# Kernel tuning notes

Hardware: AMD Instinct MI355X
Metric: run time of the kernel (lower is better)

The kernel has to match this reference:

```python
import jax, jax.numpy as jnp
import numpy as np
import math

B, H, L, DK = 2, 8, 2048, 64
SQRT_TERMS = 3  # 1 + tree + leaf_PE


def setup_inputs() -> dict:
    key = jax.random.key(0)
    ks = jax.random.split(key, 6)
    query = jax.random.normal(ks[0], (B, H, L, DK), dtype=jnp.float32)
    k = jax.random.normal(ks[1], (B, H, L, DK), dtype=jnp.float32)
    value = jax.random.normal(ks[2], (B, H, L, DK), dtype=jnp.float32)
    mask = jax.random.randint(ks[3], (B, 1, L, L), 0, 2).astype(jnp.bool_)
    tree_score = jax.random.normal(ks[4], (B, H, L, L), dtype=jnp.float32)
    leaf_score = jax.random.normal(ks[5], (B, H, L, L), dtype=jnp.float32)
    return {"query": query, "key": k, "value": value, "mask": mask,
            "tree_score": tree_score, "leaf_score": leaf_score}


def reference(query, key, value, mask, tree_score, leaf_score):
    # w_score = QK^T + tree bias + leaf bias, scaled by sqrt(3 * d_k)
    w_score = jnp.einsum('bhik,bhjk->bhij', query, key)
    w_score = (w_score + tree_score + leaf_score) / math.sqrt(SQRT_TERMS * query.shape[-1])
    # masked_fill(mask, -1e9): mask==True positions are suppressed
    w_score = jnp.where(mask, jnp.float32(-1e9), w_score)
    p_attn = jax.nn.softmax(w_score, axis=-1)
    attn_sum = jnp.einsum('bhij,bhjk->bhik', p_attn, value)
    return (attn_sum, p_attn)
```

## Files before the change

### kernel.cpp

```cpp
#include <hip/hip_runtime.h>


#define B_   2
#define H_   8
#define L_   2048
#define DK_  64
#define BH_  16
#define M_   16
#define SCALE 0.07216878364870323f
#define MASKVAL -65504.0f

typedef __attribute__((ext_vector_type(8))) short    short8;
typedef __attribute__((ext_vector_type(4))) float    f32x4;
typedef __attribute__((ext_vector_type(4))) int      i32x4;
typedef __attribute__((ext_vector_type(4))) _Float16 h16x4;
typedef __attribute__((ext_vector_type(8))) _Float16 h16x8;

__device__ __forceinline__ unsigned short f2bf(float f) {
    union { float f; unsigned int i; } x; x.f = f;
    unsigned int u = x.i;
    return (unsigned short)((u + 0x7fffu + ((u >> 16) & 1u)) >> 16);
}
__device__ __forceinline__ short8 pack8f(const float* a) {
    short8 r;
#pragma unroll
    for (int i = 0; i < 8; ++i) r[i] = (short)f2bf(a[i]);
    return r;
}
__device__ __forceinline__ int swz(int row, int colByte) {
    return (row * (L_ * 2) + colByte) ^ ((row & 7) << 4);
}

__global__ __launch_bounds__(256)
void raa_fused_kernel(const float* __restrict__ q,
                      const float* __restrict__ k,
                      const float* __restrict__ v,
                      const int*   __restrict__ mask,
                      const float* __restrict__ tree,
                      const float* __restrict__ leaf,
                      float*       __restrict__ attn,
                      float*       __restrict__ p)
{
    const int t    = threadIdx.x;
    const int wv   = t >> 6;
    const int lane = t & 63;
    const int bh   = blockIdx.x;
    const int b    = bh >> 3;
    const int i0   = blockIdx.y * M_;

    __shared__ __align__(16) unsigned short s16[M_ * L_];
    __shared__ float s_m[M_], s_linv[M_];
    char* sb = (char*)s16;

    const int prow = t >> 4;
    const int pc4  = (t & 15) * 4;

    const size_t bias_row = ((size_t)bh * L_ + i0 + prow) * L_ + pc4;
    const size_t mask_row = ((size_t)b  * L_ + i0 + prow) * L_ + pc4;
    f32x4 tB0 = __builtin_nontemporal_load((const f32x4*)(tree + bias_row));
    f32x4 lB0 = __builtin_nontemporal_load((const f32x4*)(leaf + bias_row));
    i32x4 mB0 = *(const i32x4*)(mask + mask_row);
    f32x4 tB1 = __builtin_nontemporal_load((const f32x4*)(tree + bias_row + 64));
    f32x4 lB1 = __builtin_nontemporal_load((const f32x4*)(leaf + bias_row + 64));
    i32x4 mB1 = *(const i32x4*)(mask + mask_row + 64);

    const size_t qbase = ((size_t)bh * L_ + i0 + (lane & 15)) * (size_t)DK_
                       + ((lane >> 4) * 8);
    float qf[8], qg[8];
    *(f32x4*)&qf[0] = *(const f32x4*)(q + qbase);
    *(f32x4*)&qf[4] = *(const f32x4*)(q + qbase + 4);
    *(f32x4*)&qg[0] = *(const f32x4*)(q + qbase + 32);
    *(f32x4*)&qg[4] = *(const f32x4*)(q + qbase + 36);
    const short8 aq0 = pack8f(qf), aq1 = pack8f(qg);

    const float* kbase = k + (size_t)bh * L_ * DK_ + ((lane >> 4) * 8);
    const int kr = wv * 16 + (lane & 15);
    float kc[16];
    {
        const float* kp = kbase + (size_t)kr * DK_;
        *(f32x4*)&kc[0]  = *(const f32x4*)(kp);
        *(f32x4*)&kc[4]  = *(const f32x4*)(kp + 4);
        *(f32x4*)&kc[8]  = *(const f32x4*)(kp + 32);
        *(f32x4*)&kc[12] = *(const f32x4*)(kp + 36);
    }
    for (int jc = 0; jc < 32; ++jc) {
        float kn[16];
        {
            const int nj = (jc < 31) ? jc + 1 : 31;
            const float* kp = kbase + (size_t)(nj * 64 + kr) * DK_;
            *(f32x4*)&kn[0]  = *(const f32x4*)(kp);
            *(f32x4*)&kn[4]  = *(const f32x4*)(kp + 4);
            *(f32x4*)&kn[8]  = *(const f32x4*)(kp + 32);
            *(f32x4*)&kn[12] = *(const f32x4*)(kp + 36);
        }
        const short8 kb0 = pack8f(&kc[0]);
        const short8 kb1 = pack8f(&kc[8]);
        f32x4 acc = {0.f, 0.f, 0.f, 0.f};
        acc = __builtin_amdgcn_mfma_f32_16x16x32_bf16(aq0, kb0, acc, 0, 0, 0);
        acc = __builtin_amdgcn_mfma_f32_16x16x32_bf16(aq1, kb1, acc, 0, 0, 0);
        const int r0   = (lane >> 4) * 4;
        const int ccol = jc * 64 + wv * 16 + (lane & 15);
#pragma unroll
        for (int r = 0; r < 4; ++r)
            *(_Float16*)(sb + swz(r0 + r, ccol * 2)) = (_Float16)acc[r];
#pragma unroll
        for (int u = 0; u < 16; ++u) kc[u] = kn[u];
    }
    __syncthreads();

    float m_loc = -INFINITY, l_loc = 0.f;
    auto procB = [&](int jc, f32x4 t4, f32x4 l4, i32x4 mk) {
        const int ad = swz(prow, (jc * 64 + pc4) * 2);
        h16x4 qh = *(h16x4*)(sb + ad);
        float su[4];
#pragma unroll
        for (int e = 0; e < 4; ++e) {
            float s = ((float)qh[e] + t4[e] + l4[e]) * SCALE;
            s = mk[e] ? MASKVAL : s;
            _Float16 hs = (_Float16)s;
            qh[e] = hs;
            su[e] = (float)hs;
        }
        *(h16x4*)(sb + ad) = qh;
        const float cmax = fmaxf(fmaxf(su[0], su[1]), fmaxf(su[2], su[3]));
        if (cmax > m_loc) { l_loc *= __expf(m_loc - cmax); m_loc = cmax; }
        l_loc += __expf(su[0] - m_loc) + __expf(su[1] - m_loc)
               + __expf(su[2] - m_loc) + __expf(su[3] - m_loc);
    };
    for (int jc = 0; jc < 32; jc += 2) {
        {
            const f32x4 t4 = tB0, l4 = lB0; const i32x4 mk = mB0;
            const int nj = (jc + 2 < 32) ? jc + 2 : jc;
            const size_t off = bias_row + (size_t)nj * 64;
            tB0 = __builtin_nontemporal_load((const f32x4*)(tree + off));
            lB0 = __builtin_nontemporal_load((const f32x4*)(leaf + off));
            mB0 = *(const i32x4*)(mask + mask_row + (size_t)nj * 64);
            procB(jc, t4, l4, mk);
        }
        {
            const f32x4 t4 = tB1, l4 = lB1; const i32x4 mk = mB1;
            const int nj = (jc + 3 < 32) ? jc + 3 : jc + 1;
            const size_t off = bias_row + (size_t)nj * 64;
            tB1 = __builtin_nontemporal_load((const f32x4*)(tree + off));
            lB1 = __builtin_nontemporal_load((const f32x4*)(leaf + off));
            mB1 = *(const i32x4*)(mask + mask_row + (size_t)nj * 64);
            procB(jc + 1, t4, l4, mk);
        }
    }
#pragma unroll
    for (int d = 1; d < 16; d <<= 1) {
        const float mo = __shfl_xor(m_loc, d);
        const float lo = __shfl_xor(l_loc, d);
        const float mn = fmaxf(m_loc, mo);
        l_loc = l_loc * __expf(m_loc - mn) + lo * __expf(mo - mn);
        m_loc = mn;
    }
    if ((t & 15) == 0) { s_m[prow] = m_loc; s_linv[prow] = 1.f / l_loc; }
    __syncthreads();

    {
        const float mrow = s_m[prow], li = s_linv[prow];
        const size_t prowoff = ((size_t)bh * L_ + i0 + prow) * L_;
        const int c8 = (t & 15) * 8;
        for (int ch = 0; ch < 16; ++ch) {
            const int col = ch * 128 + c8;
            const int ad  = swz(prow, col * 2);
            const h16x8 hv = *(const h16x8*)(sb + ad);
            float pv[8];
#pragma unroll
            for (int e = 0; e < 8; ++e) pv[e] = __expf((float)hv[e] - mrow) * li;
            f32x4 o0 = { pv[0], pv[1], pv[2], pv[3] };
            f32x4 o1 = { pv[4], pv[5], pv[6], pv[7] };
            __builtin_nontemporal_store(o0, (f32x4*)(p + prowoff + col));
            __builtin_nontemporal_store(o1, (f32x4*)(p + prowoff + col + 4));
            *(short8*)(sb + ad) = pack8f(pv);
        }
    }
    __syncthreads();

    f32x4 oacc = {0.f, 0.f, 0.f, 0.f};
    const float* vb = v + (size_t)bh * L_ * DK_ + wv * 16 + (lane & 15);
#pragma unroll 2
    for (int ch = 0; ch < 16; ++ch) {
#pragma unroll
        for (int kk = 0; kk < 4; ++kk) {
            const int jb = ch * 128 + kk * 32 + (lane >> 4) * 8;
            const short8 af = *(const short8*)(sb + swz(lane & 15, jb * 2));
            const float* vp = vb + (size_t)jb * DK_;
            float vf[8];
#pragma unroll
            for (int u = 0; u < 8; ++u) vf[u] = vp[(size_t)u * DK_];
            const short8 bfr = pack8f(vf);
            oacc = __builtin_amdgcn_mfma_f32_16x16x32_bf16(af, bfr, oacc, 0, 0, 0);
        }
    }
    {
        const int r0  = (lane >> 4) * 4;
        const int col = wv * 16 + (lane & 15);
#pragma unroll
        for (int r = 0; r < 4; ++r)
            attn[((size_t)bh * L_ + i0 + r0 + r) * DK_ + col] = oacc[r];
    }
}

extern "C" void kernel_launch(void* const* d_in, const int* in_sizes, int n_in,
                              void* d_out, int out_size, void* d_ws, size_t ws_size,
                              hipStream_t stream) {
    const float* q    = (const float*)d_in[0];
    const float* k    = (const float*)d_in[1];
    const float* v    = (const float*)d_in[2];
    const int*   mask = (const int*)d_in[3];
    const float* tree = (const float*)d_in[4];
    const float* leaf = (const float*)d_in[5];

    float* attn = (float*)d_out;
    float* p    = attn + (size_t)B_ * H_ * L_ * DK_;

    dim3 grid(BH_, L_ / M_);
    raa_fused_kernel<<<grid, 256, 0, stream>>>(q, k, v, mask, tree, leaf, attn, p);
}
```

Before: 790.3 us.

## Halve query rows per block and pre-convert K/V to bf16 in workspace

Each block now handles 8 query rows instead of 16, which halves shared memory per block and doubles the grid. It also raises the launch-bounds occupancy hint to 4 blocks. When workspace is available, a separate pre-pass converts K and V to bf16 so the fused kernel reads half-size operands and skips per-block repacking. The cost is that each K/V tile is reread by twice as many blocks, half of every MFMA's rows go unused, and there is an extra kernel launch.

```diff
diff --git a/kernel.cpp b/kernel.cpp
--- a/kernel.cpp
+++ b/kernel.cpp
@@ -6,7 +6,7 @@
 #define L_   2048
 #define DK_  64
 #define BH_  16
-#define M_   16
+#define M_   8
 #define SCALE 0.07216878364870323f
 #define MASKVAL -65504.0f
 
@@ -32,9 +32,25 @@
 }
 
 __global__ __launch_bounds__(256)
+void cvt_kv_bf16(const float* __restrict__ k, const float* __restrict__ v,
+                 unsigned short* __restrict__ out) {
+    const size_t N = (size_t)B_ * H_ * L_ * DK_;
+    const size_t stride = (size_t)gridDim.x * blockDim.x * 8;
+    for (size_t i = ((size_t)blockIdx.x * blockDim.x + threadIdx.x) * 8;
+         i < 2 * N; i += stride) {
+        const float* src = (i < N) ? (k + i) : (v + (i - N));
+        float a[8];
+        *(f32x4*)&a[0] = *(const f32x4*)(src);
+        *(f32x4*)&a[4] = *(const f32x4*)(src + 4);
+        *(short8*)(out + i) = pack8f(a);
+    }
+}
+
+template<bool BF>
+__global__ __launch_bounds__(256, 4)
 void raa_fused_kernel(const float* __restrict__ q,
-                      const float* __restrict__ k,
-                      const float* __restrict__ v,
+                      const void*  __restrict__ kptr,
+                      const void*  __restrict__ vptr,
                       const int*   __restrict__ mask,
                       const float* __restrict__ tree,
                       const float* __restrict__ leaf,
@@ -52,20 +68,21 @@
     __shared__ float s_m[M_], s_linv[M_];
     char* sb = (char*)s16;
 
-    const int prow = t >> 4;
-    const int pc4  = (t & 15) * 4;
+    const int prow = t >> 5;
+    const int lr   = t & 31;
+    const int pc4  = lr * 4;
 
     const size_t bias_row = ((size_t)bh * L_ + i0 + prow) * L_ + pc4;
     const size_t mask_row = ((size_t)b  * L_ + i0 + prow) * L_ + pc4;
     f32x4 tB0 = __builtin_nontemporal_load((const f32x4*)(tree + bias_row));
     f32x4 lB0 = __builtin_nontemporal_load((const f32x4*)(leaf + bias_row));
     i32x4 mB0 = *(const i32x4*)(mask + mask_row);
-    f32x4 tB1 = __builtin_nontemporal_load((const f32x4*)(tree + bias_row + 64));
-    f32x4 lB1 = __builtin_nontemporal_load((const f32x4*)(leaf + bias_row + 64));
-    i32x4 mB1 = *(const i32x4*)(mask + mask_row + 64);
-
-    const size_t qbase = ((size_t)bh * L_ + i0 + (lane & 15)) * (size_t)DK_
-                       + ((lane >> 4) * 8);
+    f32x4 tB1 = __builtin_nontemporal_load((const f32x4*)(tree + bias_row + 128));
+    f32x4 lB1 = __builtin_nontemporal_load((const f32x4*)(leaf + bias_row + 128));
+    i32x4 mB1 = *(const i32x4*)(mask + mask_row + 128);
+
+    const int qrow = (i0 + (lane & 15) < L_) ? i0 + (lane & 15) : L_ - 1;
+    const size_t qbase = ((size_t)bh * L_ + qrow) * (size_t)DK_ + ((lane >> 4) * 8);
     float qf[8], qg[8];
     *(f32x4*)&qf[0] = *(const f32x4*)(q + qbase);
     *(f32x4*)&qf[4] = *(const f32x4*)(q + qbase + 4);
@@ -73,44 +90,77 @@
     *(f32x4*)&qg[4] = *(const f32x4*)(q + qbase + 36);
     const short8 aq0 = pack8f(qf), aq1 = pack8f(qg);
 
-    const float* kbase = k + (size_t)bh * L_ * DK_ + ((lane >> 4) * 8);
     const int kr = wv * 16 + (lane & 15);
-    float kc[16];
-    {
-        const float* kp = kbase + (size_t)kr * DK_;
-        *(f32x4*)&kc[0]  = *(const f32x4*)(kp);
-        *(f32x4*)&kc[4]  = *(const f32x4*)(kp + 4);
-        *(f32x4*)&kc[8]  = *(const f32x4*)(kp + 32);
-        *(f32x4*)&kc[12] = *(const f32x4*)(kp + 36);
-    }
-    for (int jc = 0; jc < 32; ++jc) {
-        float kn[16];
+    const int r0 = (lane >> 4) * 4;
+    if constexpr (BF) {
+        const unsigned short* kb16 = (const unsigned short*)kptr
+                                   + (size_t)bh * L_ * DK_ + ((lane >> 4) * 8);
+        short8 kc0, kc1;
         {
-            const int nj = (jc < 31) ? jc + 1 : 31;
-            const float* kp = kbase + (size_t)(nj * 64 + kr) * DK_;
-            *(f32x4*)&kn[0]  = *(const f32x4*)(kp);
-            *(f32x4*)&kn[4]  = *(const f32x4*)(kp + 4);
-            *(f32x4*)&kn[8]  = *(const f32x4*)(kp + 32);
-            *(f32x4*)&kn[12] = *(const f32x4*)(kp + 36);
-        }
-        const short8 kb0 = pack8f(&kc[0]);
-        const short8 kb1 = pack8f(&kc[8]);
-        f32x4 acc = {0.f, 0.f, 0.f, 0.f};
-        acc = __builtin_amdgcn_mfma_f32_16x16x32_bf16(aq0, kb0, acc, 0, 0, 0);
-        acc = __builtin_amdgcn_mfma_f32_16x16x32_bf16(aq1, kb1, acc, 0, 0, 0);
-        const int r0   = (lane >> 4) * 4;
-        const int ccol = jc * 64 + wv * 16 + (lane & 15);
-#pragma unroll
-        for (int r = 0; r < 4; ++r)
-            *(_Float16*)(sb + swz(r0 + r, ccol * 2)) = (_Float16)acc[r];
-#pragma unroll
-        for (int u = 0; u < 16; ++u) kc[u] = kn[u];
+            const unsigned short* kp = kb16 + (size_t)kr * DK_;
+            kc0 = *(const short8*)(kp);
+            kc1 = *(const short8*)(kp + 32);
+        }
+        for (int jc = 0; jc < 32; ++jc) {
+            short8 kn0, kn1;
+            {
+                const int nj = (jc < 31) ? jc + 1 : 31;
+                const unsigned short* kp = kb16 + (size_t)(nj * 64 + kr) * DK_;
+                kn0 = *(const short8*)(kp);
+                kn1 = *(const short8*)(kp + 32);
+            }
+            f32x4 acc = {0.f, 0.f, 0.f, 0.f};
+            acc = __builtin_amdgcn_mfma_f32_16x16x32_bf16(aq0, kc0, acc, 0, 0, 0);
+            acc = __builtin_amdgcn_mfma_f32_16x16x32_bf16(aq1, kc1, acc, 0, 0, 0);
+            const int ccol = jc * 64 + wv * 16 + (lane & 15);
+            if (r0 < M_) {
+#pragma unroll
+                for (int r = 0; r < 4; ++r)
+                    *(_Float16*)(sb + swz(r0 + r, ccol * 2)) = (_Float16)acc[r];
+            }
+            kc0 = kn0; kc1 = kn1;
+        }
+    } else {
+        const float* kbase = (const float*)kptr + (size_t)bh * L_ * DK_
+                           + ((lane >> 4) * 8);
+        float kc[16];
+        {
+            const float* kp = kbase + (size_t)kr * DK_;
+            *(f32x4*)&kc[0]  = *(const f32x4*)(kp);
+            *(f32x4*)&kc[4]  = *(const f32x4*)(kp + 4);
+            *(f32x4*)&kc[8]  = *(const f32x4*)(kp + 32);
+            *(f32x4*)&kc[12] = *(const f32x4*)(kp + 36);
+        }
+        for (int jc = 0; jc < 32; ++jc) {
+            float kn[16];
+            {
+                const int nj = (jc < 31) ? jc + 1 : 31;
+                const float* kp = kbase + (size_t)(nj * 64 + kr) * DK_;
+                *(f32x4*)&kn[0]  = *(const f32x4*)(kp);
+                *(f32x4*)&kn[4]  = *(const f32x4*)(kp + 4);
+                *(f32x4*)&kn[8]  = *(const f32x4*)(kp + 32);
+                *(f32x4*)&kn[12] = *(const f32x4*)(kp + 36);
+            }
+            const short8 kb0 = pack8f(&kc[0]);
+            const short8 kb1 = pack8f(&kc[8]);
+            f32x4 acc = {0.f, 0.f, 0.f, 0.f};
+            acc = __builtin_amdgcn_mfma_f32_16x16x32_bf16(aq0, kb0, acc, 0, 0, 0);
+            acc = __builtin_amdgcn_mfma_f32_16x16x32_bf16(aq1, kb1, acc, 0, 0, 0);
+            const int ccol = jc * 64 + wv * 16 + (lane & 15);
+            if (r0 < M_) {
+#pragma unroll
+                for (int r = 0; r < 4; ++r)
+                    *(_Float16*)(sb + swz(r0 + r, ccol * 2)) = (_Float16)acc[r];
+            }
+#pragma unroll
+            for (int u = 0; u < 16; ++u) kc[u] = kn[u];
+        }
     }
     __syncthreads();
 
     float m_loc = -INFINITY, l_loc = 0.f;
     auto procB = [&](int jc, f32x4 t4, f32x4 l4, i32x4 mk) {
-        const int ad = swz(prow, (jc * 64 + pc4) * 2);
+        const int ad = swz(prow, (jc * 128 + pc4) * 2);
         h16x4 qh = *(h16x4*)(sb + ad);
         float su[4];
 #pragma unroll
@@ -127,43 +177,43 @@
         l_loc += __expf(su[0] - m_loc) + __expf(su[1] - m_loc)
                + __expf(su[2] - m_loc) + __expf(su[3] - m_loc);
     };
-    for (int jc = 0; jc < 32; jc += 2) {
+    for (int jc = 0; jc < 16; jc += 2) {
         {
             const f32x4 t4 = tB0, l4 = lB0; const i32x4 mk = mB0;
-            const int nj = (jc + 2 < 32) ? jc + 2 : jc;
-            const size_t off = bias_row + (size_t)nj * 64;
+            const int nj = (jc + 2 < 16) ? jc + 2 : jc;
+            const size_t off = bias_row + (size_t)nj * 128;
             tB0 = __builtin_nontemporal_load((const f32x4*)(tree + off));
             lB0 = __builtin_nontemporal_load((const f32x4*)(leaf + off));
-            mB0 = *(const i32x4*)(mask + mask_row + (size_t)nj * 64);
+            mB0 = *(const i32x4*)(mask + mask_row + (size_t)nj * 128);
             procB(jc, t4, l4, mk);
         }
         {
             const f32x4 t4 = tB1, l4 = lB1; const i32x4 mk = mB1;
-            const int nj = (jc + 3 < 32) ? jc + 3 : jc + 1;
-            const size_t off = bias_row + (size_t)nj * 64;
+            const int nj = (jc + 3 < 16) ? jc + 3 : jc + 1;
+            const size_t off = bias_row + (size_t)nj * 128;
             tB1 = __builtin_nontemporal_load((const f32x4*)(tree + off));
             lB1 = __builtin_nontemporal_load((const f32x4*)(leaf + off));
-            mB1 = *(const i32x4*)(mask + mask_row + (size_t)nj * 64);
+            mB1 = *(const i32x4*)(mask + mask_row + (size_t)nj * 128);
             procB(jc + 1, t4, l4, mk);
         }
     }
 #pragma unroll
-    for (int d = 1; d < 16; d <<= 1) {
+    for (int d = 1; d < 32; d <<= 1) {
         const float mo = __shfl_xor(m_loc, d);
         const float lo = __shfl_xor(l_loc, d);
         const float mn = fmaxf(m_loc, mo);
         l_loc = l_loc * __expf(m_loc - mn) + lo * __expf(mo - mn);
         m_loc = mn;
     }
-    if ((t & 15) == 0) { s_m[prow] = m_loc; s_linv[prow] = 1.f / l_loc; }
+    if (lr == 0) { s_m[prow] = m_loc; s_linv[prow] = 1.f / l_loc; }
     __syncthreads();
 
     {
         const float mrow = s_m[prow], li = s_linv[prow];
         const size_t prowoff = ((size_t)bh * L_ + i0 + prow) * L_;
-        const int c8 = (t & 15) * 8;
-        for (int ch = 0; ch < 16; ++ch) {
-            const int col = ch * 128 + c8;
+        const int c8 = lr * 8;
+        for (int ch = 0; ch < 8; ++ch) {
+            const int col = ch * 256 + c8;
             const int ad  = swz(prow, col * 2);
             const h16x8 hv = *(const h16x8*)(sb + ad);
             float pv[8];
@@ -179,27 +229,47 @@
     __syncthreads();
 
     f32x4 oacc = {0.f, 0.f, 0.f, 0.f};
-    const float* vb = v + (size_t)bh * L_ * DK_ + wv * 16 + (lane & 15);
+    if constexpr (BF) {
+        const unsigned short* vb16 = (const unsigned short*)vptr
+                                   + (size_t)bh * L_ * DK_ + wv * 16 + (lane & 15);
 #pragma unroll 2
-    for (int ch = 0; ch < 16; ++ch) {
-#pragma unroll
-        for (int kk = 0; kk < 4; ++kk) {
-            const int jb = ch * 128 + kk * 32 + (lane >> 4) * 8;
-            const short8 af = *(const short8*)(sb + swz(lane & 15, jb * 2));
-            const float* vp = vb + (size_t)jb * DK_;
-            float vf[8];
-#pragma unroll
-            for (int u = 0; u < 8; ++u) vf[u] = vp[(size_t)u * DK_];
-            const short8 bfr = pack8f(vf);
-            oacc = __builtin_amdgcn_mfma_f32_16x16x32_bf16(af, bfr, oacc, 0, 0, 0);
+        for (int ch = 0; ch < 16; ++ch) {
+#pragma unroll
+            for (int kk = 0; kk < 4; ++kk) {
+                const int jb = ch * 128 + kk * 32 + (lane >> 4) * 8;
+                const short8 af = *(const short8*)(sb + swz(lane & 7, jb * 2));
+                const unsigned short* vp = vb16 + (size_t)jb * DK_;
+                short8 bfr;
+#pragma unroll
+                for (int u = 0; u < 8; ++u) bfr[u] = (short)vp[(size_t)u * DK_];
+                oacc = __builtin_amdgcn_mfma_f32_16x16x32_bf16(af, bfr, oacc, 0, 0, 0);
+            }
+        }
+    } else {
+        const float* vb = (const float*)vptr + (size_t)bh * L_ * DK_
+                        + wv * 16 + (lane & 15);
+#pragma unroll 2
+        for (int ch = 0; ch < 16; ++ch) {
+#pragma unroll
+            for (int kk = 0; kk < 4; ++kk) {
+                const int jb = ch * 128 + kk * 32 + (lane >> 4) * 8;
+                const short8 af = *(const short8*)(sb + swz(lane & 7, jb * 2));
+                const float* vp = vb + (size_t)jb * DK_;
+                float vf[8];
+#pragma unroll
+                for (int u = 0; u < 8; ++u) vf[u] = vp[(size_t)u * DK_];
+                const short8 bfr = pack8f(vf);
+                oacc = __builtin_amdgcn_mfma_f32_16x16x32_bf16(af, bfr, oacc, 0, 0, 0);
+            }
         }
     }
     {
-        const int r0  = (lane >> 4) * 4;
-        const int col = wv * 16 + (lane & 15);
-#pragma unroll
-        for (int r = 0; r < 4; ++r)
-            attn[((size_t)bh * L_ + i0 + r0 + r) * DK_ + col] = oacc[r];
+        if (r0 < M_) {
+            const int col = wv * 16 + (lane & 15);
+#pragma unroll
+            for (int r = 0; r < 4; ++r)
+                attn[((size_t)bh * L_ + i0 + r0 + r) * DK_ + col] = oacc[r];
+        }
     }
 }
 
@@ -216,6 +286,17 @@
     float* attn = (float*)d_out;
     float* p    = attn + (size_t)B_ * H_ * L_ * DK_;
 
+    const size_t N    = (size_t)B_ * H_ * L_ * DK_;
+    const size_t need = 2 * N * sizeof(unsigned short);
+
     dim3 grid(BH_, L_ / M_);
-    raa_fused_kernel<<<grid, 256, 0, stream>>>(q, k, v, mask, tree, leaf, attn, p);
-}
+    if (d_ws != nullptr && ws_size >= need) {
+        unsigned short* kv16 = (unsigned short*)d_ws;
+        cvt_kv_bf16<<<2048, 256, 0, stream>>>(k, v, kv16);
+        raa_fused_kernel<true><<<grid, 256, 0, stream>>>(
+            q, kv16, kv16 + N, mask, tree, leaf, attn, p);
+    } else {
+        raa_fused_kernel<false><<<grid, 256, 0, stream>>>(
+            q, k, v, mask, tree, leaf, attn, p);
+    }
+}
```

Result: slower. 817.1 us (+3.4%).
